# Kernel tuning notes

Hardware: AMD Instinct MI355X
Metric: run time of the kernel (lower is better)

Reference implementation:

```python
import jax, jax.numpy as jnp
import numpy as np
from jax import lax

STRIDE = 1
PADDING = 4
Q = 5


def setup_inputs() -> dict:
    key = jax.random.key(0)
    k1, k2, k3 = jax.random.split(key, 3)
    B, C_in, T = 16, 128, 8192
    C_out, K = 256, 9
    x = jax.random.normal(k1, (B, C_in, T), dtype=jnp.float32)
    fan_in = C_in * K
    std = np.sqrt(2.0 / fan_in).astype(np.float32)
    conv_weights = jax.random.normal(k2, (C_out, C_in, K, Q), dtype=jnp.float32) * std
    # init matches _initialize_weights' operator_probs pattern plus small noise
    operator_probs = jnp.concatenate(
        [jnp.full((C_out, 1), 1.5), jnp.full((C_out, Q - 1), 0.25)], axis=1
    ) + 0.01 * jax.random.normal(k3, (C_out, Q), dtype=jnp.float32)
    return {"x": x, "conv_weights": conv_weights, "operator_probs": operator_probs}


def _selfonn_forward(x, conv_weights, operator_probs):
    # Fuse the q parallel convs into one conv with q*C_out output channels.
    C_out, C_in, K, q = conv_weights.shape
    # (O, I, K, q) -> (q, O, I, K) -> (q*O, I, K); q-major output channel order
    w = jnp.transpose(conv_weights, (3, 0, 1, 2)).reshape(q * C_out, C_in, K)
    z = lax.conv_general_dilated(
        x, w,
        window_strides=(STRIDE,),
        padding=[(PADDING, PADDING)],
        dimension_numbers=("NCH", "OIH", "NCH"),
    )  # (B, q*C_out, T_out)
    B = x.shape[0]
    T_out = z.shape[-1]
    z = z.reshape(B, q, C_out, T_out)
    # per-branch nonlinearities: identity, sin, cos, tanh, clamped exp
    outs = jnp.stack(
        [
            z[:, 0],
            jnp.sin(z[:, 1]),
            jnp.cos(z[:, 2]),
            jnp.tanh(z[:, 3]),
            jnp.exp(jnp.clip(z[:, 4], -8.0, 8.0)),
        ],
        axis=-1,
    )  # (B, C_out, T_out, q)
    op_w = jax.nn.softmax(operator_probs, axis=1)  # (C_out, q)
    return jnp.einsum("bctq,cq->bct", outs, op_w)


def reference(x, conv_weights, operator_probs):
    return _selfonn_forward(x, conv_weights, operator_probs)
```

## Files before the change

kernel.cpp:

```cpp
#include <hip/hip_runtime.h>

#define CI   128
#define TT   8192
#define CO   256
#define KW   9
#define NQ   5
#define PADL 4
#define KDIM (CI*KW)
#define NSTEP 36
#define NF (NQ*NSTEP)
#define BCO  128
#define BT   128
#define XROWS 136
#define XPITCH 136
#define WSLOT 4096

typedef __attribute__((ext_vector_type(8))) short short8;
typedef __attribute__((ext_vector_type(4))) float float4v;
typedef __attribute__((address_space(1))) const unsigned int ga_u32;
typedef __attribute__((address_space(3))) unsigned int la_u32;

static __device__ __forceinline__ short f2bf(float f) {
  union { float f; unsigned u; } c; c.f = f;
  unsigned u = c.u;
  return (short)((u + 0x7FFFu + ((u >> 16) & 1u)) >> 16);
}

static __device__ __forceinline__ float tanh_fast(float z) {
  float e = __expf(2.f * z);
  return (e - 1.f) / (e + 1.f);
}

static __device__ __forceinline__ void gload_lds16(const short* g, short* l) {
  __builtin_amdgcn_global_load_lds((ga_u32*)g, (la_u32*)l, 16, 0, 0);
}

__global__ void selfonn_wtrans(const float* __restrict__ w, short* __restrict__ wT, int n) {
  int o = blockIdx.x * 256 + threadIdx.x;
  if (o >= n) return;
  int ci = o & (CI - 1);
  int k  = (o >> 7) % KW;
  int co = (o / KDIM) & (CO - 1);
  int q  = o / (KDIM * CO);
  wT[o] = f2bf(w[((co * CI + ci) * KW + k) * NQ + q]);
}

__global__ __launch_bounds__(256, 2) void selfonn_main(
    const float* __restrict__ x, const short* __restrict__ wT,
    const float* __restrict__ probs, float* __restrict__ out) {

  __shared__ __align__(16) short xs[XROWS][XPITCH];
  __shared__ __align__(16) short ws[4][WSLOT];
  __shared__ float opw[BCO][NQ];

  const int tid  = threadIdx.x;
  const int lane = tid & 63;
  const int wid  = tid >> 6;
  const int wm   = wid >> 1;
  const int wt   = wid & 1;
  const int l15  = lane & 15;
  const int lg   = lane >> 4;
  const int b    = blockIdx.z;
  const int co0  = blockIdx.y * BCO;
  const int t0   = blockIdx.x * BT;

  if (tid < BCO) {
    float p[NQ];
    float mx = -1e30f;
    #pragma unroll
    for (int j = 0; j < NQ; ++j) { p[j] = probs[(co0 + tid) * NQ + j]; mx = fmaxf(mx, p[j]); }
    float s = 0.f;
    #pragma unroll
    for (int j = 0; j < NQ; ++j) { p[j] = __expf(p[j] - mx); s += p[j]; }
    float inv = 1.0f / s;
    #pragma unroll
    for (int j = 0; j < NQ; ++j) opw[tid][j] = p[j] * inv;
  }

  int soff0, soff1;
  {
    int G0 = tid, G1 = 256 + tid;
    soff0 = (G0 >> 2) * KDIM + (((G0 - (G0 >> 3)) & 3) << 3);
    soff1 = (G1 >> 2) * KDIM + (((G1 - (G1 >> 3)) & 3) << 3);
  }
  const int sdst0 = (wid * 64) * 8;
  const int sdst1 = (256 + wid * 64) * 8;
  const short* wTb = wT + (size_t)co0 * KDIM;

  #pragma unroll
  for (int ps = 0; ps < 3; ++ps) {
    gload_lds16(wTb + ps * 32 + soff0, &ws[ps][0] + sdst0);
    gload_lds16(wTb + ps * 32 + soff1, &ws[ps][0] + sdst1);
  }

  const float* xb = x + (size_t)b * CI * TT;
  #pragma unroll
  for (int it = 0; it < 17; ++it) {
    int cell = tid + it * 256;
    int ci = cell & (CI - 1);
    int tc = cell >> 7;
    int tg = t0 - PADL + tc * 4;
    float4v v = {0.f, 0.f, 0.f, 0.f};
    if (tg >= 0 && tg <= TT - 4)
      v = *(const float4v*)(xb + (size_t)ci * TT + tg);
    int tl = tc * 4;
    xs[tl + 0][ci] = f2bf(v[0]);
    xs[tl + 1][ci] = f2bf(v[1]);
    xs[tl + 2][ci] = f2bf(v[2]);
    xs[tl + 3][ci] = f2bf(v[3]);
  }

  int afo[4], bfo[4];
  #pragma unroll
  for (int m = 0; m < 4; ++m) {
    int co = wm * 64 + m * 16 + l15;
    afo[m] = co * 32 + (((lg + (co >> 1)) & 3) << 3);
  }
  #pragma unroll
  for (int n = 0; n < 4; ++n)
    bfo[n] = (wt * 64 + n * 16 + l15) * XPITCH + (lg << 3);

  float4v oacc[4][4];
  float4v acc[4][4];
  #pragma unroll
  for (int m = 0; m < 4; ++m)
    #pragma unroll
    for (int n = 0; n < 4; ++n) {
      oacc[m][n] = (float4v){0.f, 0.f, 0.f, 0.f};
      acc[m][n]  = (float4v){0.f, 0.f, 0.f, 0.f};
    }

  __syncthreads();

  int sq = 0, q = 0;
  int s_step = 3, s_qoff = 0;

  #define BODY(SLOT, SSLOT, DOEPI, DOSTAGE, VMASM)                     \
    {                                                                  \
                                                \
      const short* wb = &ws[SLOT][0];                                  \
      const short* xp = &xs[0][0] + (sq >> 2) * XPITCH + ((sq & 3) << 5); \
      short8 af[4], bf[4];                                             \
      _Pragma("unroll") for (int m = 0; m < 4; ++m)                    \
        af[m] = *(const short8*)(wb + afo[m]);                         \
      _Pragma("unroll") for (int n = 0; n < 4; ++n)                    \
        bf[n] = *(const short8*)(xp + bfo[n]);                         \
                                                   \
      if (DOSTAGE) {                                                   \
        const short* wp = wTb + s_qoff + s_step * 32;                  \
        gload_lds16(wp + soff0, &ws[SSLOT][0] + sdst0);                \
        gload_lds16(wp + soff1, &ws[SSLOT][0] + sdst1);                \
        if (++s_step == NSTEP) { s_step = 0; s_qoff += CO * KDIM; }    \
      }                                                                \
                                             \
      asm volatile(VMASM ::: "memory");                                \
                                                               \
      __builtin_amdgcn_s_barrier();                                    \
                   \
      __builtin_amdgcn_s_setprio(1);                                   \
      _Pragma("unroll") for (int m = 0; m < 4; ++m)                    \
        _Pragma("unroll") for (int n = 0; n < 4; ++n)                  \
          acc[m][n] = __builtin_amdgcn_mfma_f32_16x16x32_bf16(         \
              af[m], bf[n], acc[m][n], 0, 0, 0);                       \
      __builtin_amdgcn_s_setprio(0);                                   \
                                        \
      if (DOEPI && sq == NSTEP - 1) {                                  \
        _Pragma("unroll") for (int m = 0; m < 4; ++m) {                \
          _Pragma("unroll") for (int jj = 0; jj < 4; ++jj) {           \
            int co_l = wm * 64 + m * 16 + lg * 4 + jj;                 \
            float wqv = opw[co_l][q];                                  \
            _Pragma("unroll") for (int n = 0; n < 4; ++n) {            \
              float z = acc[m][n][jj];                                 \
              float f;                                                 \
              if (q == 0)      f = z;                                  \
              else if (q == 1) f = __sinf(z);                          \
              else if (q == 2) f = __cosf(z);                          \
              else if (q == 3) f = tanh_fast(z);                       \
              else             f = __expf(fminf(fmaxf(z, -8.f), 8.f)); \
              oacc[m][n][jj] += wqv * f;                               \
              acc[m][n][jj] = 0.f;                                     \
            }                                                          \
          }                                                            \
        }                                                              \
        ++q; sq = 0;                                                   \
      } else {                                                         \
        ++sq;                                                          \
      }                                                                \
                                                               \
      __builtin_amdgcn_s_barrier();                                    \
    }

  for (int u = 0; u < 44; ++u) {
    BODY(0, 3, 0, 1, "s_waitcnt vmcnt(4)")
    BODY(1, 0, 0, 1, "s_waitcnt vmcnt(4)")
    BODY(2, 1, 0, 1, "s_waitcnt vmcnt(4)")
    BODY(3, 2, 1, 1, "s_waitcnt vmcnt(4)")
  }
  BODY(0, 3, 0, 1, "s_waitcnt vmcnt(4)")
  BODY(1, 0, 0, 0, "s_waitcnt vmcnt(2)")
  BODY(2, 1, 0, 0, "s_waitcnt vmcnt(0)")
  BODY(3, 2, 1, 0, "s_waitcnt vmcnt(0)")
  #undef BODY

  float* ob = out + (size_t)(b * CO + co0) * TT;
  #pragma unroll
  for (int m = 0; m < 4; ++m) {
    #pragma unroll
    for (int jj = 0; jj < 4; ++jj) {
      int co_l = wm * 64 + m * 16 + lg * 4 + jj;
      int tcol = t0 + wt * 64 + l15;
      float* orow = ob + (size_t)co_l * TT + tcol;
      #pragma unroll
      for (int n = 0; n < 4; ++n)
        orow[n * 16] = oacc[m][n][jj];
    }
  }
}

extern "C" void kernel_launch(void* const* d_in, const int* in_sizes, int n_in,
                              void* d_out, int out_size, void* d_ws, size_t ws_size,
                              hipStream_t stream) {
  const float* x     = (const float*)d_in[0];
  const float* w     = (const float*)d_in[1];
  const float* probs = (const float*)d_in[2];
  float* out = (float*)d_out;
  short* wT  = (short*)d_ws;

  int nw = NQ * CO * KDIM;
  selfonn_wtrans<<<dim3((nw + 255) / 256), 256, 0, stream>>>(w, wT, nw);

  dim3 grid(TT / BT, CO / BCO, 16);
  selfonn_main<<<grid, 256, 0, stream>>>(x, wT, probs, out);
}
```

Baseline: 380.5 us.

## Double-buffer MFMA operand fragments to prefetch next step's LDS reads

```diff
diff --git a/kernel.cpp b/kernel.cpp
--- a/kernel.cpp
+++ b/kernel.cpp
@@ -132,19 +132,17 @@
 
   __syncthreads();
 
+  short8 afA[4], bfA[4], afB[4], bfB[4];
+  #pragma unroll
+  for (int m = 0; m < 4; ++m) afA[m] = *(const short8*)(&ws[0][0] + afo[m]);
+  #pragma unroll
+  for (int n = 0; n < 4; ++n) bfA[n] = *(const short8*)(&xs[0][0] + bfo[n]);
+
   int sq = 0, q = 0;
   int s_step = 3, s_qoff = 0;
 
-  #define BODY(SLOT, SSLOT, DOEPI, DOSTAGE, VMASM)                     \
+  #define BODY(RSLOT, SSLOT, DOEPI, DOSTAGE, VMASM, CAF, CBF, NAF, NBF) \
     {                                                                  \
-                                                \
-      const short* wb = &ws[SLOT][0];                                  \
-      const short* xp = &xs[0][0] + (sq >> 2) * XPITCH + ((sq & 3) << 5); \
-      short8 af[4], bf[4];                                             \
-      _Pragma("unroll") for (int m = 0; m < 4; ++m)                    \
-        af[m] = *(const short8*)(wb + afo[m]);                         \
-      _Pragma("unroll") for (int n = 0; n < 4; ++n)                    \
-        bf[n] = *(const short8*)(xp + bfo[n]);                         \
                                                    \
       if (DOSTAGE) {                                                   \
         const short* wp = wTb + s_qoff + s_step * 32;                  \
@@ -152,16 +150,28 @@
         gload_lds16(wp + soff1, &ws[SSLOT][0] + sdst1);                \
         if (++s_step == NSTEP) { s_step = 0; s_qoff += CO * KDIM; }    \
       }                                                                \
-                                             \
+                    \
       asm volatile(VMASM ::: "memory");                                \
-                                                               \
+                            \
       __builtin_amdgcn_s_barrier();                                    \
-                   \
+      __builtin_amdgcn_sched_barrier(0);                               \
+                \
+      {                                                                \
+        int sqn = (sq == NSTEP - 1) ? 0 : sq + 1;                      \
+        const short* nb = &ws[RSLOT][0];                               \
+        _Pragma("unroll") for (int m = 0; m < 4; ++m)                  \
+          NAF[m] = *(const short8*)(nb + afo[m]);                      \
+        const short* xp = &xs[0][0] + (sqn >> 2) * XPITCH + ((sqn & 3) << 5); \
+        _Pragma("unroll") for (int n = 0; n < 4; ++n)                  \
+          NBF[n] = *(const short8*)(xp + bfo[n]);                      \
+      }                                                                \
+      __builtin_amdgcn_sched_barrier(0);                               \
+             \
       __builtin_amdgcn_s_setprio(1);                                   \
       _Pragma("unroll") for (int m = 0; m < 4; ++m)                    \
         _Pragma("unroll") for (int n = 0; n < 4; ++n)                  \
           acc[m][n] = __builtin_amdgcn_mfma_f32_16x16x32_bf16(         \
-              af[m], bf[n], acc[m][n], 0, 0, 0);                       \
+              CAF[m], CBF[n], acc[m][n], 0, 0, 0);                     \
       __builtin_amdgcn_s_setprio(0);                                   \
                                         \
       if (DOEPI && sq == NSTEP - 1) {                                  \
@@ -186,20 +196,20 @@
       } else {                                                         \
         ++sq;                                                          \
       }                                                                \
-                                                               \
+       \
       __builtin_amdgcn_s_barrier();                                    \
     }
 
   for (int u = 0; u < 44; ++u) {
-    BODY(0, 3, 0, 1, "s_waitcnt vmcnt(4)")
-    BODY(1, 0, 0, 1, "s_waitcnt vmcnt(4)")
-    BODY(2, 1, 0, 1, "s_waitcnt vmcnt(4)")
-    BODY(3, 2, 1, 1, "s_waitcnt vmcnt(4)")
-  }
-  BODY(0, 3, 0, 1, "s_waitcnt vmcnt(4)")
-  BODY(1, 0, 0, 0, "s_waitcnt vmcnt(2)")
-  BODY(2, 1, 0, 0, "s_waitcnt vmcnt(0)")
-  BODY(3, 2, 1, 0, "s_waitcnt vmcnt(0)")
+    BODY(1, 3, 0, 1, "s_waitcnt vmcnt(4)", afA, bfA, afB, bfB)
+    BODY(2, 0, 0, 1, "s_waitcnt vmcnt(4)", afB, bfB, afA, bfA)
+    BODY(3, 1, 0, 1, "s_waitcnt vmcnt(4)", afA, bfA, afB, bfB)
+    BODY(0, 2, 1, 1, "s_waitcnt vmcnt(4)", afB, bfB, afA, bfA)
+  }
+  BODY(1, 3, 0, 1, "s_waitcnt vmcnt(4)", afA, bfA, afB, bfB)
+  BODY(2, 0, 0, 0, "s_waitcnt vmcnt(2)", afB, bfB, afA, bfA)
+  BODY(3, 1, 0, 0, "s_waitcnt vmcnt(0)", afA, bfA, afB, bfB)
+  BODY(0, 2, 1, 0, "s_waitcnt vmcnt(0)", afB, bfB, afA, bfA)
   #undef BODY
 
   float* ob = out + (size_t)(b * CO + co0) * TT;
```

New measurement: 410.8 us. 1.08x slower.

## Load pre-packed weight fragments directly into registers, drop LDS weight staging and barriers

Applied to the files above, without the earlier changes.

```diff
diff --git a/kernel.cpp b/kernel.cpp
--- a/kernel.cpp
+++ b/kernel.cpp
@@ -13,12 +13,9 @@
 #define BT   128
 #define XROWS 136
 #define XPITCH 136
-#define WSLOT 4096
 
 typedef __attribute__((ext_vector_type(8))) short short8;
 typedef __attribute__((ext_vector_type(4))) float float4v;
-typedef __attribute__((address_space(1))) const unsigned int ga_u32;
-typedef __attribute__((address_space(3))) unsigned int la_u32;
 
 static __device__ __forceinline__ short f2bf(float f) {
   union { float f; unsigned u; } c; c.f = f;
@@ -31,26 +28,32 @@
   return (e - 1.f) / (e + 1.f);
 }
 
-static __device__ __forceinline__ void gload_lds16(const short* g, short* l) {
-  __builtin_amdgcn_global_load_lds((ga_u32*)g, (la_u32*)l, 16, 0, 0);
-}
-
-__global__ void selfonn_wtrans(const float* __restrict__ w, short* __restrict__ wT, int n) {
+__global__ void selfonn_wpack(const float* __restrict__ w, short* __restrict__ wpk, int n) {
   int o = blockIdx.x * 256 + threadIdx.x;
   if (o >= n) return;
-  int ci = o & (CI - 1);
-  int k  = (o >> 7) % KW;
-  int co = (o / KDIM) & (CO - 1);
-  int q  = o / (KDIM * CO);
-  wT[o] = f2bf(w[((co * CI + ci) * KW + k) * NQ + q]);
+  int j    = o & 7;
+  int lane = (o >> 3) & 63;
+  int m    = (o >> 9) & 3;
+  int wm   = (o >> 11) & 1;
+  int ft   = o >> 12;
+  int ch   = ft / NF;
+  int fi   = ft - ch * NF;
+  int q    = fi / NSTEP;
+  int step = fi - q * NSTEP;
+  int k    = step >> 2;
+  int cib  = step & 3;
+  int l15  = lane & 15;
+  int lg   = lane >> 4;
+  int co   = ch * 128 + wm * 64 + m * 16 + l15;
+  int ci   = cib * 32 + lg * 8 + j;
+  wpk[o] = f2bf(w[((co * CI + ci) * KW + k) * NQ + q]);
 }
 
 __global__ __launch_bounds__(256, 2) void selfonn_main(
-    const float* __restrict__ x, const short* __restrict__ wT,
+    const float* __restrict__ x, const short* __restrict__ wpk,
     const float* __restrict__ probs, float* __restrict__ out) {
 
   __shared__ __align__(16) short xs[XROWS][XPITCH];
-  __shared__ __align__(16) short ws[4][WSLOT];
   __shared__ float opw[BCO][NQ];
 
   const int tid  = threadIdx.x;
@@ -61,7 +64,8 @@
   const int l15  = lane & 15;
   const int lg   = lane >> 4;
   const int b    = blockIdx.z;
-  const int co0  = blockIdx.y * BCO;
+  const int ch   = blockIdx.y;
+  const int co0  = ch * BCO;
   const int t0   = blockIdx.x * BT;
 
   if (tid < BCO) {
@@ -75,22 +79,6 @@
     float inv = 1.0f / s;
     #pragma unroll
     for (int j = 0; j < NQ; ++j) opw[tid][j] = p[j] * inv;
-  }
-
-  int soff0, soff1;
-  {
-    int G0 = tid, G1 = 256 + tid;
-    soff0 = (G0 >> 2) * KDIM + (((G0 - (G0 >> 3)) & 3) << 3);
-    soff1 = (G1 >> 2) * KDIM + (((G1 - (G1 >> 3)) & 3) << 3);
-  }
-  const int sdst0 = (wid * 64) * 8;
-  const int sdst1 = (256 + wid * 64) * 8;
-  const short* wTb = wT + (size_t)co0 * KDIM;
-
-  #pragma unroll
-  for (int ps = 0; ps < 3; ++ps) {
-    gload_lds16(wTb + ps * 32 + soff0, &ws[ps][0] + sdst0);
-    gload_lds16(wTb + ps * 32 + soff1, &ws[ps][0] + sdst1);
   }
 
   const float* xb = x + (size_t)b * CI * TT;
@@ -110,15 +98,12 @@
     xs[tl + 3][ci] = f2bf(v[3]);
   }
 
-  int afo[4], bfo[4];
-  #pragma unroll
-  for (int m = 0; m < 4; ++m) {
-    int co = wm * 64 + m * 16 + l15;
-    afo[m] = co * 32 + (((lg + (co >> 1)) & 3) << 3);
-  }
+  int bfo[4];
   #pragma unroll
   for (int n = 0; n < 4; ++n)
     bfo[n] = (wt * 64 + n * 16 + l15) * XPITCH + (lg << 3);
+
+  const short* wp = wpk + ((size_t)(ch * NF) * 2 + wm) * 2048 + lane * 8;
 
   float4v oacc[4][4];
   float4v acc[4][4];
@@ -132,38 +117,33 @@
 
   __syncthreads();
 
+  short8 WA[4], WB[4], BA[4], BB[4];
+  #pragma unroll
+  for (int m = 0; m < 4; ++m) WA[m] = *(const short8*)(wp + m * 512);
+  #pragma unroll
+  for (int n = 0; n < 4; ++n) BA[n] = *(const short8*)(&xs[0][0] + bfo[n]);
+
   int sq = 0, q = 0;
-  int s_step = 3, s_qoff = 0;
-
-  #define BODY(SLOT, SSLOT, DOEPI, DOSTAGE, VMASM)                     \
+
+  #define STEP(CW, CB, NW, NB, DOPF, DOEPI)                            \
     {                                                                  \
-                                                \
-      const short* wb = &ws[SLOT][0];                                  \
-      const short* xp = &xs[0][0] + (sq >> 2) * XPITCH + ((sq & 3) << 5); \
-      short8 af[4], bf[4];                                             \
-      _Pragma("unroll") for (int m = 0; m < 4; ++m)                    \
-        af[m] = *(const short8*)(wb + afo[m]);                         \
-      _Pragma("unroll") for (int n = 0; n < 4; ++n)                    \
-        bf[n] = *(const short8*)(xp + bfo[n]);                         \
-                                                   \
-      if (DOSTAGE) {                                                   \
-        const short* wp = wTb + s_qoff + s_step * 32;                  \
-        gload_lds16(wp + soff0, &ws[SSLOT][0] + sdst0);                \
-        gload_lds16(wp + soff1, &ws[SSLOT][0] + sdst1);                \
-        if (++s_step == NSTEP) { s_step = 0; s_qoff += CO * KDIM; }    \
+      if (DOPF) {                                                      \
+          \
+        wp += 4096;                                                    \
+        _Pragma("unroll") for (int m = 0; m < 4; ++m)                  \
+          NW[m] = *(const short8*)(wp + m * 512);                      \
+                            \
+        int sqn = (sq == NSTEP - 1) ? 0 : sq + 1;                      \
+        const short* xp = &xs[0][0] + (sqn >> 2) * XPITCH + ((sqn & 3) << 5); \
+        _Pragma("unroll") for (int n = 0; n < 4; ++n)                  \
+          NB[n] = *(const short8*)(xp + bfo[n]);                       \
       }                                                                \
-                                             \
-      asm volatile(VMASM ::: "memory");                                \
-                                                               \
-      __builtin_amdgcn_s_barrier();                                    \
-                   \
       __builtin_amdgcn_s_setprio(1);                                   \
       _Pragma("unroll") for (int m = 0; m < 4; ++m)                    \
         _Pragma("unroll") for (int n = 0; n < 4; ++n)                  \
           acc[m][n] = __builtin_amdgcn_mfma_f32_16x16x32_bf16(         \
-              af[m], bf[n], acc[m][n], 0, 0, 0);                       \
+              CW[m], CB[n], acc[m][n], 0, 0, 0);                       \
       __builtin_amdgcn_s_setprio(0);                                   \
-                                        \
       if (DOEPI && sq == NSTEP - 1) {                                  \
         _Pragma("unroll") for (int m = 0; m < 4; ++m) {                \
           _Pragma("unroll") for (int jj = 0; jj < 4; ++jj) {           \
@@ -186,21 +166,15 @@
       } else {                                                         \
         ++sq;                                                          \
       }                                                                \
-                                                               \
-      __builtin_amdgcn_s_barrier();                                    \
     }
 
-  for (int u = 0; u < 44; ++u) {
-    BODY(0, 3, 0, 1, "s_waitcnt vmcnt(4)")
-    BODY(1, 0, 0, 1, "s_waitcnt vmcnt(4)")
-    BODY(2, 1, 0, 1, "s_waitcnt vmcnt(4)")
-    BODY(3, 2, 1, 1, "s_waitcnt vmcnt(4)")
-  }
-  BODY(0, 3, 0, 1, "s_waitcnt vmcnt(4)")
-  BODY(1, 0, 0, 0, "s_waitcnt vmcnt(2)")
-  BODY(2, 1, 0, 0, "s_waitcnt vmcnt(0)")
-  BODY(3, 2, 1, 0, "s_waitcnt vmcnt(0)")
-  #undef BODY
+  for (int u = 0; u < 89; ++u) {
+    STEP(WA, BA, WB, BB, 1, 0)
+    STEP(WB, BB, WA, BA, 1, 1)
+  }
+  STEP(WA, BA, WB, BB, 1, 0)
+  STEP(WB, BB, WA, BA, 0, 1)
+  #undef STEP
 
   float* ob = out + (size_t)(b * CO + co0) * TT;
   #pragma unroll
@@ -224,11 +198,11 @@
   const float* w     = (const float*)d_in[1];
   const float* probs = (const float*)d_in[2];
   float* out = (float*)d_out;
-  short* wT  = (short*)d_ws;
+  short* wpk = (short*)d_ws;
 
   int nw = NQ * CO * KDIM;
-  selfonn_wtrans<<<dim3((nw + 255) / 256), 256, 0, stream>>>(w, wT, nw);
+  selfonn_wpack<<<dim3((nw + 255) / 256), 256, 0, stream>>>(w, wpk, nw);
 
   dim3 grid(TT / BT, CO / BCO, 16);
-  selfonn_main<<<grid, 256, 0, stream>>>(x, wT, probs, out);
-}
+  selfonn_main<<<grid, 256, 0, stream>>>(x, wpk, probs, out);
+}
```

Measured after the change: 352.6 us. 7.3% less time.
